# Performance work log

Hardware: AMD Instinct MI355X
Metric: run time of the kernel (lower is better)

## Reference

```python
import jax, jax.numpy as jnp
import numpy as np
from jax import lax

W_BCE, W_DICE, W_FT, W_HD = 1.0, 1.0, 1.0, 0.1
TV_ALPHA, TV_BETA, TV_GAMMA = 0.7, 0.3, 0.75
HD_MAX_DIST, HD_BK = 10, 3
SMOOTH, EPS, HD_EPS = 1e-6, 1e-7, 1e-8


def _max_pool(x, k):
    # torch F.max_pool2d pads with -inf implicitly
    pad = k // 2
    return lax.reduce_window(x, -jnp.inf, lax.max, (1, 1, k, k), (1, 1, 1, 1),
                             [(0, 0), (0, 0), (pad, pad), (pad, pad)])


def _min_pool(x, k):
    pad = k // 2
    return lax.reduce_window(x, jnp.inf, lax.min, (1, 1, k, k), (1, 1, 1, 1),
                             [(0, 0), (0, 0), (pad, pad), (pad, pad)])


def _soft_boundary(mask, k):
    dil = _max_pool(mask, k)
    ero = _min_pool(mask, k)  # == -max_pool(-mask)
    return jnp.maximum(dil - ero, 0.0)


def _bce_with_logits(logits, target):
    # numerically stable: max(x,0) - x*t + log1p(exp(-|x|))
    return jnp.mean(jnp.maximum(logits, 0.0) - logits * target +
                    jnp.log1p(jnp.exp(-jnp.abs(logits))))


def _dice_loss(probs, target):
    p = probs.reshape(probs.shape[0], -1)
    t = target.reshape(target.shape[0], -1)
    inter = jnp.sum(p * t, axis=1)
    denom = jnp.sum(p, axis=1) + jnp.sum(t, axis=1)
    dice = (2.0 * inter + SMOOTH) / (denom + SMOOTH + EPS)
    return jnp.mean(1.0 - dice)


def _focal_tversky(probs, target):
    p = probs.reshape(probs.shape[0], -1)
    t = target.reshape(target.shape[0], -1)
    TP = jnp.sum(p * t, axis=1)
    FP = jnp.sum(p * (1.0 - t), axis=1)
    FN = jnp.sum((1.0 - p) * t, axis=1)
    tv = (TP + SMOOTH) / (TP + TV_ALPHA * FP + TV_BETA * FN + SMOOTH + EPS)
    return jnp.mean(jnp.power(1.0 - tv, TV_GAMMA))


def _hausdorff_surrogate(probs, target):
    pred_b = _soft_boundary(probs, HD_BK)
    gt_b = _soft_boundary(target, HD_BK)
    total = jnp.zeros((), probs.dtype)
    weight_sum = 0.0
    for d in range(1, HD_MAX_DIST + 1):
        pred_d = _max_pool(pred_b, 2 * d + 1)
        gt_d = _max_pool(gt_b, 2 * d + 1)
        w = float(d) / float(HD_MAX_DIST)
        total = total + w * (jnp.mean(jnp.abs(pred_d - gt_b)) +
                             jnp.mean(jnp.abs(gt_d - pred_b)))
        weight_sum += w
    return total / (weight_sum + HD_EPS)


def setup_inputs() -> dict:
    key = jax.random.key(0)
    k1, k2 = jax.random.split(key)
    B, C, H, W = 16, 1, 512, 512
    logits = jax.random.normal(k1, (B, C, H, W), dtype=jnp.float32)
    target = jax.random.randint(k2, (B, C, H, W), 0, 2, dtype=jnp.int32)
    return {"logits": logits, "target": target}


def reference(logits, target):
    t = target.astype(jnp.float32)
    bce = _bce_with_logits(logits, t)
    probs = jax.nn.sigmoid(logits)
    d = _dice_loss(probs, t)
    ft = _focal_tversky(probs, t)
    hd = _hausdorff_surrogate(probs, t)
    return W_BCE * bce + W_DICE * d + W_FT * ft + W_HD * hd
```

## Files before the change

kernel.cpp:

```cpp
#include <hip/hip_runtime.h>
#include <math.h>

namespace {

constexpr int B = 16, H = 512, W = 512;
constexpr int HWc = H * W;
constexpr size_t Nc = (size_t)B * HWc;

constexpr int NSTRIP = 13;
constexpr int CENT = 42;
constexpr int NBAND = 16;
constexpr int NWORK = NSTRIP * NBAND * B * 2;
constexpr int NSB = NWORK / 4;
constexpr int NBCE = B * 64;

template <int CTRL>
__device__ __forceinline__ float dpp_shift1(float v) {
  int i = __float_as_int(v);
  int r = __builtin_amdgcn_update_dpp(i, i, CTRL, 0xF, 0xF, false);
  return __int_as_float(r);
}

__device__ __forceinline__ float hmax3(float v) {
  return fmaxf(fmaxf(dpp_shift1<0x138>(v), v), dpp_shift1<0x130>(v));
}
__device__ __forceinline__ void hminmax3(float v, float& mx, float& mn) {
  float s1 = dpp_shift1<0x138>(v);
  float s2 = dpp_shift1<0x130>(v);
  mx = fmaxf(fmaxf(s1, v), s2);
  mn = fminf(fminf(s1, v), s2);
}

__device__ __forceinline__ float wave_sum(float v) {
#pragma unroll
  for (int off = 32; off > 0; off >>= 1) v += __shfl_down(v, off);
  return v;
}

__device__ __forceinline__ float block_reduce_256(float v, float* sm, int tid) {
#pragma unroll
  for (int off = 32; off > 0; off >>= 1) v += __shfl_down(v, off);
  int lane = tid & 63, wid = tid >> 6;
  if (lane == 0) sm[wid] = v;
  __syncthreads();
  float r = 0.f;
  if (tid == 0) r = sm[0] + sm[1] + sm[2] + sm[3];
  __syncthreads();
  return r;
}

template <int CH>
__device__ __forceinline__ float load_src(const float* __restrict__ Lg,
                                          const int* __restrict__ Tg, int gy,
                                          int colc) {
  gy = min(max(gy, 0), H - 1);
  if constexpr (CH == 0) {
    float x = Lg[gy * W + colc];
    float e = __expf(-x);
    return __builtin_amdgcn_rcpf(1.f + e);
  } else {
    return (float)Tg[gy * W + colc];
  }
}

template <int D>
__device__ __forceinline__ void dilate_steps(float (&a)[52],
                                             const float (&o)[32],
                                             float (&accv)[4]) {
  if constexpr (D <= 10) {
    float hp = hmax3(a[D - 1]);
    float hc = hmax3(a[D]);
#pragma unroll
    for (int r = D; r <= 51 - D; ++r) {
      float hn = hmax3(a[r + 1]);
      float nv = fmaxf(fmaxf(hp, hc), hn);
      hp = hc;
      hc = hn;
      a[r] = nv;
    }
    constexpr float wd = 0.1f * (float)D;
#pragma unroll
    for (int k = 0; k < 32; ++k) accv[k & 3] += wd * fabsf(a[10 + k] - o[k]);
    dilate_steps<D + 1>(a, o, accv);
  }
}

template <int CH>
__device__ __forceinline__ void fused_body(const float* __restrict__ Lg,
                                           const int* __restrict__ Tg,
                                           int lane, int strip, int band,
                                           int bz,
                                           float* __restrict__ chain_p) {
  int col = strip * CENT - 11 + lane;
  int colc = min(max(col, 0), W - 1);
  int y0 = band * 32;

  float o[32];
  {
    float v0 = load_src<1 - CH>(Lg, Tg, y0 - 1, colc);
    float v1 = load_src<1 - CH>(Lg, Tg, y0, colc);
    float hx0, hn0, hx1, hn1;
    hminmax3(v0, hx0, hn0);
    hminmax3(v1, hx1, hn1);
#pragma unroll
    for (int k = 0; k < 32; ++k) {
      float v2 = load_src<1 - CH>(Lg, Tg, y0 + 1 + k, colc);
      float hx2, hn2;
      hminmax3(v2, hx2, hn2);
      o[k] = fmaxf(fmaxf(hx0, hx1), hx2) - fminf(fminf(hn0, hn1), hn2);
      hx0 = hx1;
      hx1 = hx2;
      hn0 = hn1;
      hn1 = hn2;
    }
  }

  float a[52];
  {
    float v0 = load_src<CH>(Lg, Tg, y0 - 11, colc);
    float v1 = load_src<CH>(Lg, Tg, y0 - 10, colc);
    float hx0, hn0, hx1, hn1;
    hminmax3(v0, hx0, hn0);
    hminmax3(v1, hx1, hn1);
#pragma unroll
    for (int r = 0; r < 52; ++r) {
      float v2 = load_src<CH>(Lg, Tg, y0 - 9 + r, colc);
      float hx2, hn2;
      hminmax3(v2, hx2, hn2);
      a[r] = fmaxf(fmaxf(hx0, hx1), hx2) - fminf(fminf(hn0, hn1), hn2);
      hx0 = hx1;
      hx1 = hx2;
      hn0 = hn1;
      hn1 = hn2;
    }
  }

  float accv[4] = {0.f, 0.f, 0.f, 0.f};
  dilate_steps<1>(a, o, accv);
  float acc = (accv[0] + accv[1]) + (accv[2] + accv[3]);

  bool valid = (lane >= 11 && lane <= 52 && col < W);
  acc = valid ? acc : 0.f;
  acc = wave_sum(acc);
  if (lane == 0) chain_p[(bz * NBAND + band) * NSTRIP + strip] = acc;
}

__device__ __forceinline__ void bce_body(const float* __restrict__ logits,
                                         const int* __restrict__ target,
                                         int blk, float* __restrict__ bceA,
                                         float* __restrict__ spA,
                                         float* __restrict__ stA,
                                         float* __restrict__ sptA) {
  __shared__ float smr[4];
  int img = blk >> 6, seg = blk & 63;
  const float4* L4 =
      (const float4*)(logits + (size_t)img * HWc + (size_t)seg * 4096);
  const int4* T4 =
      (const int4*)(target + (size_t)img * HWc + (size_t)seg * 4096);
  int tid = threadIdx.x;
  float s_bce = 0.f, s_p = 0.f, s_t = 0.f, s_pt = 0.f;
#pragma unroll
  for (int it = 0; it < 4; ++it) {
    float4 x4 = L4[it * 256 + tid];
    int4 t4 = T4[it * 256 + tid];
    float xs[4] = {x4.x, x4.y, x4.z, x4.w};
    int ts[4] = {t4.x, t4.y, t4.z, t4.w};
#pragma unroll
    for (int j = 0; j < 4; ++j) {
      float x = xs[j];
      float tf = (float)ts[j];
      float e = __expf(-x);
      float p = __builtin_amdgcn_rcpf(1.f + e);
      s_p += p;
      s_t += tf;
      s_pt += p * tf;
      s_bce += x * (1.f - tf) + __logf(1.f + e);
    }
  }
  float r;
  r = block_reduce_256(s_bce, smr, tid);
  if (tid == 0) bceA[blk] = r;
  r = block_reduce_256(s_p, smr, tid);
  if (tid == 0) spA[blk] = r;
  r = block_reduce_256(s_t, smr, tid);
  if (tid == 0) stA[blk] = r;
  r = block_reduce_256(s_pt, smr, tid);
  if (tid == 0) sptA[blk] = r;
}

__global__ void __launch_bounds__(256, 4) fused_kernel(
    const float* __restrict__ logits, const int* __restrict__ target,
    float* __restrict__ bceA, float* __restrict__ spA,
    float* __restrict__ stA, float* __restrict__ sptA,
    float* __restrict__ chain_p) {
  if (blockIdx.x < NBCE) {
    bce_body(logits, target, blockIdx.x, bceA, spA, stA, sptA);
    return;
  }
  int tid = threadIdx.x;
  int lane = tid & 63;
  int wv = __builtin_amdgcn_readfirstlane(tid >> 6);
  int widx = (blockIdx.x - NBCE) * 4 + wv;
  int strip = widx % NSTRIP;
  int rest = widx / NSTRIP;
  int band = rest & 15;
  int bz = rest >> 4;
  int img = bz & 15, chain = bz >> 4;
  const float* Lg = logits + (size_t)img * HWc;
  const int* Tg = target + (size_t)img * HWc;
  if (chain == 0)
    fused_body<0>(Lg, Tg, lane, strip, band, bz, chain_p);
  else
    fused_body<1>(Lg, Tg, lane, strip, band, bz, chain_p);
}

__global__ void finalize_kernel(const float* __restrict__ bceA,
                                const float* __restrict__ spA,
                                const float* __restrict__ stA,
                                const float* __restrict__ sptA,
                                const float* __restrict__ chain_p,
                                float* __restrict__ out) {
  __shared__ float smr[4];
  __shared__ float smImg[16][3];
  __shared__ double smd[16][2];
  int tid = threadIdx.x;

  float s = 0.f;
  for (int i = tid; i < NBCE; i += 256) s += bceA[i];
  float bce_sum = block_reduce_256(s, smr, tid);

  s = 0.f;
  for (int i = tid; i < NWORK; i += 256) s += chain_p[i];
  float hd_sum = block_reduce_256(s, smr, tid);

  {
    int img = tid >> 4, part = tid & 15;
    float sp = 0.f, st = 0.f, spt = 0.f;
    for (int j = part; j < 64; j += 16) {
      int idx = img * 64 + j;
      sp += spA[idx];
      st += stA[idx];
      spt += sptA[idx];
    }
#pragma unroll
    for (int off = 8; off > 0; off >>= 1) {
      sp += __shfl_down(sp, off, 16);
      st += __shfl_down(st, off, 16);
      spt += __shfl_down(spt, off, 16);
    }
    if (part == 0) {
      smImg[img][0] = sp;
      smImg[img][1] = st;
      smImg[img][2] = spt;
    }
  }
  __syncthreads();
  if (tid < 16) {
    double sp = smImg[tid][0], st = smImg[tid][1], spt = smImg[tid][2];
    double dice = (2.0 * spt + 1e-6) / (sp + st + 1e-6 + 1e-7);
    double tv = (spt + 1e-6) /
                (spt + 0.7 * (sp - spt) + 0.3 * (st - spt) + 1e-6 + 1e-7);
    smd[tid][0] = 1.0 - dice;
    smd[tid][1] = pow(1.0 - tv, 0.75);
  }
  __syncthreads();
  if (tid == 0) {
    double dice_l = 0.0, ft_l = 0.0;
    for (int i = 0; i < 16; ++i) {
      dice_l += smd[i][0];
      ft_l += smd[i][1];
    }
    dice_l /= 16.0;
    ft_l /= 16.0;
    const double Nd = (double)Nc;
    double bce = (double)bce_sum / Nd;
    double hd = ((double)hd_sum / Nd) / (5.5 + 1e-8);
    out[0] = (float)(bce + dice_l + ft_l + 0.1 * hd);
  }
}

}

extern "C" void kernel_launch(void* const* d_in, const int* in_sizes, int n_in,
                              void* d_out, int out_size, void* d_ws,
                              size_t ws_size, hipStream_t stream) {
  const float* logits = (const float*)d_in[0];
  const int* target = (const int*)d_in[1];
  float* out = (float*)d_out;

  float* part = (float*)d_ws;
  float* bceA = part;
  float* spA = part + NBCE;
  float* stA = part + 2 * NBCE;
  float* sptA = part + 3 * NBCE;
  float* chain_p = part + 4 * NBCE;

  fused_kernel<<<dim3(NBCE + NSB), dim3(256), 0, stream>>>(
      logits, target, bceA, spA, stA, sptA, chain_p);
  finalize_kernel<<<1, 256, 0, stream>>>(bceA, spA, stA, sptA, chain_p, out);
}
```

Before: 136.6 us.

## Use bit-packed binary morphology for target boundary dilation chain

Measured after the change: 119.4 us. 1.14x faster.

```diff
diff --git a/kernel.cpp b/kernel.cpp
--- a/kernel.cpp
+++ b/kernel.cpp
@@ -14,12 +14,18 @@
 constexpr int NSB = NWORK / 4;
 constexpr int NBCE = B * 64;
 
+
 template <int CTRL>
 __device__ __forceinline__ float dpp_shift1(float v) {
   int i = __float_as_int(v);
   int r = __builtin_amdgcn_update_dpp(i, i, CTRL, 0xF, 0xF, false);
   return __int_as_float(r);
 }
+template <int CTRL>
+__device__ __forceinline__ unsigned dpp_shift1u(unsigned v) {
+  return (unsigned)__builtin_amdgcn_update_dpp((int)v, (int)v, CTRL, 0xF, 0xF,
+                                               false);
+}
 
 __device__ __forceinline__ float hmax3(float v) {
   return fmaxf(fmaxf(dpp_shift1<0x138>(v), v), dpp_shift1<0x130>(v));
@@ -29,6 +35,19 @@
   float s2 = dpp_shift1<0x130>(v);
   mx = fmaxf(fmaxf(s1, v), s2);
   mn = fminf(fminf(s1, v), s2);
+}
+
+__device__ __forceinline__ unsigned long long or3_lanes(unsigned long long v) {
+  unsigned lo = (unsigned)v, hi = (unsigned)(v >> 32);
+  unsigned rlo = dpp_shift1u<0x138>(lo) | lo | dpp_shift1u<0x130>(lo);
+  unsigned rhi = dpp_shift1u<0x138>(hi) | hi | dpp_shift1u<0x130>(hi);
+  return ((unsigned long long)rhi << 32) | rlo;
+}
+__device__ __forceinline__ unsigned long long and3_lanes(unsigned long long v) {
+  unsigned lo = (unsigned)v, hi = (unsigned)(v >> 32);
+  unsigned rlo = dpp_shift1u<0x138>(lo) & lo & dpp_shift1u<0x130>(lo);
+  unsigned rhi = dpp_shift1u<0x138>(hi) & hi & dpp_shift1u<0x130>(hi);
+  return ((unsigned long long)rhi << 32) | rlo;
 }
 
 __device__ __forceinline__ float wave_sum(float v) {
@@ -85,26 +104,25 @@
   }
 }
 
-template <int CH>
-__device__ __forceinline__ void fused_body(const float* __restrict__ Lg,
-                                           const int* __restrict__ Tg,
-                                           int lane, int strip, int band,
-                                           int bz,
-                                           float* __restrict__ chain_p) {
+__device__ __forceinline__ void fused_body0(const float* __restrict__ Lg,
+                                            const int* __restrict__ Tg,
+                                            int lane, int strip, int band,
+                                            int bz,
+                                            float* __restrict__ chain_p) {
   int col = strip * CENT - 11 + lane;
   int colc = min(max(col, 0), W - 1);
   int y0 = band * 32;
 
   float o[32];
   {
-    float v0 = load_src<1 - CH>(Lg, Tg, y0 - 1, colc);
-    float v1 = load_src<1 - CH>(Lg, Tg, y0, colc);
+    float v0 = load_src<1>(Lg, Tg, y0 - 1, colc);
+    float v1 = load_src<1>(Lg, Tg, y0, colc);
     float hx0, hn0, hx1, hn1;
     hminmax3(v0, hx0, hn0);
     hminmax3(v1, hx1, hn1);
 #pragma unroll
     for (int k = 0; k < 32; ++k) {
-      float v2 = load_src<1 - CH>(Lg, Tg, y0 + 1 + k, colc);
+      float v2 = load_src<1>(Lg, Tg, y0 + 1 + k, colc);
       float hx2, hn2;
       hminmax3(v2, hx2, hn2);
       o[k] = fmaxf(fmaxf(hx0, hx1), hx2) - fminf(fminf(hn0, hn1), hn2);
@@ -117,14 +135,14 @@
 
   float a[52];
   {
-    float v0 = load_src<CH>(Lg, Tg, y0 - 11, colc);
-    float v1 = load_src<CH>(Lg, Tg, y0 - 10, colc);
+    float v0 = load_src<0>(Lg, Tg, y0 - 11, colc);
+    float v1 = load_src<0>(Lg, Tg, y0 - 10, colc);
     float hx0, hn0, hx1, hn1;
     hminmax3(v0, hx0, hn0);
     hminmax3(v1, hx1, hn1);
 #pragma unroll
     for (int r = 0; r < 52; ++r) {
-      float v2 = load_src<CH>(Lg, Tg, y0 - 9 + r, colc);
+      float v2 = load_src<0>(Lg, Tg, y0 - 9 + r, colc);
       float hx2, hn2;
       hminmax3(v2, hx2, hn2);
       a[r] = fmaxf(fmaxf(hx0, hx1), hx2) - fminf(fminf(hn0, hn1), hn2);
@@ -145,13 +163,74 @@
   if (lane == 0) chain_p[(bz * NBAND + band) * NSTRIP + strip] = acc;
 }
 
+__device__ __forceinline__ void fused_body1(const float* __restrict__ Lg,
+                                            const int* __restrict__ Tg,
+                                            int lane, int strip, int band,
+                                            int bz,
+                                            float* __restrict__ chain_p) {
+  int col = strip * CENT - 11 + lane;
+  int colc = min(max(col, 0), W - 1);
+  int y0 = band * 32;
+
+  float o[32];
+  {
+    float v0 = load_src<0>(Lg, Tg, y0 - 1, colc);
+    float v1 = load_src<0>(Lg, Tg, y0, colc);
+    float hx0, hn0, hx1, hn1;
+    hminmax3(v0, hx0, hn0);
+    hminmax3(v1, hx1, hn1);
+#pragma unroll
+    for (int k = 0; k < 32; ++k) {
+      float v2 = load_src<0>(Lg, Tg, y0 + 1 + k, colc);
+      float hx2, hn2;
+      hminmax3(v2, hx2, hn2);
+      o[k] = fmaxf(fmaxf(hx0, hx1), hx2) - fminf(fminf(hn0, hn1), hn2);
+      hx0 = hx1;
+      hx1 = hx2;
+      hn0 = hn1;
+      hn1 = hn2;
+    }
+  }
+
+  unsigned long long tb = 0ull;
+#pragma unroll
+  for (int j = 0; j < 54; ++j) {
+    int gy = min(max(y0 - 11 + j, 0), H - 1);
+    tb |= (unsigned long long)(unsigned)Tg[gy * W + colc] << j;
+  }
+
+  unsigned long long vd = tb | (tb << 1) | (tb >> 1);
+  unsigned long long ve = tb & (tb << 1) & (tb >> 1);
+  unsigned long long ab = (or3_lanes(vd) & ~and3_lanes(ve)) >> 1;
+
+  float accv[4] = {0.f, 0.f, 0.f, 0.f};
+#pragma unroll
+  for (int d = 1; d <= 10; ++d) {
+    unsigned long long s = ab | (ab << 1) | (ab >> 1);
+    ab = or3_lanes(s);
+    const float wd = 0.1f * (float)d;
+    unsigned lo = (unsigned)ab, hi = (unsigned)(ab >> 32);
+#pragma unroll
+    for (int k = 0; k < 32; ++k) {
+      unsigned bit =
+          (k < 22) ? ((lo >> (10 + k)) & 1u) : ((hi >> (k - 22)) & 1u);
+      accv[k & 3] += wd * fabsf((float)bit - o[k]);
+    }
+  }
+  float acc = (accv[0] + accv[1]) + (accv[2] + accv[3]);
+
+  bool valid = (lane >= 11 && lane <= 52 && col < W);
+  acc = valid ? acc : 0.f;
+  acc = wave_sum(acc);
+  if (lane == 0) chain_p[(bz * NBAND + band) * NSTRIP + strip] = acc;
+}
+
 __device__ __forceinline__ void bce_body(const float* __restrict__ logits,
                                          const int* __restrict__ target,
                                          int blk, float* __restrict__ bceA,
                                          float* __restrict__ spA,
                                          float* __restrict__ stA,
-                                         float* __restrict__ sptA) {
-  __shared__ float smr[4];
+                                         float* __restrict__ sptA, float* sm) {
   int img = blk >> 6, seg = blk & 63;
   const float4* L4 =
       (const float4*)(logits + (size_t)img * HWc + (size_t)seg * 4096);
@@ -178,13 +257,13 @@
     }
   }
   float r;
-  r = block_reduce_256(s_bce, smr, tid);
+  r = block_reduce_256(s_bce, sm, tid);
   if (tid == 0) bceA[blk] = r;
-  r = block_reduce_256(s_p, smr, tid);
+  r = block_reduce_256(s_p, sm, tid);
   if (tid == 0) spA[blk] = r;
-  r = block_reduce_256(s_t, smr, tid);
+  r = block_reduce_256(s_t, sm, tid);
   if (tid == 0) stA[blk] = r;
-  r = block_reduce_256(s_pt, smr, tid);
+  r = block_reduce_256(s_pt, sm, tid);
   if (tid == 0) sptA[blk] = r;
 }
 
@@ -193,11 +272,12 @@
     float* __restrict__ bceA, float* __restrict__ spA,
     float* __restrict__ stA, float* __restrict__ sptA,
     float* __restrict__ chain_p) {
+  __shared__ float smr[4];
+  int tid = threadIdx.x;
   if (blockIdx.x < NBCE) {
-    bce_body(logits, target, blockIdx.x, bceA, spA, stA, sptA);
+    bce_body(logits, target, blockIdx.x, bceA, spA, stA, sptA, smr);
     return;
   }
-  int tid = threadIdx.x;
   int lane = tid & 63;
   int wv = __builtin_amdgcn_readfirstlane(tid >> 6);
   int widx = (blockIdx.x - NBCE) * 4 + wv;
@@ -209,9 +289,9 @@
   const float* Lg = logits + (size_t)img * HWc;
   const int* Tg = target + (size_t)img * HWc;
   if (chain == 0)
-    fused_body<0>(Lg, Tg, lane, strip, band, bz, chain_p);
+    fused_body0(Lg, Tg, lane, strip, band, bz, chain_p);
   else
-    fused_body<1>(Lg, Tg, lane, strip, band, bz, chain_p);
+    fused_body1(Lg, Tg, lane, strip, band, bz, chain_p);
 }
 
 __global__ void finalize_kernel(const float* __restrict__ bceA,
@@ -226,11 +306,23 @@
   int tid = threadIdx.x;
 
   float s = 0.f;
-  for (int i = tid; i < NBCE; i += 256) s += bceA[i];
+  {
+    const float4* b4 = (const float4*)bceA;
+    for (int i = tid; i < NBCE / 4; i += 256) {
+      float4 v = b4[i];
+      s += (v.x + v.y) + (v.z + v.w);
+    }
+  }
   float bce_sum = block_reduce_256(s, smr, tid);
 
   s = 0.f;
-  for (int i = tid; i < NWORK; i += 256) s += chain_p[i];
+  {
+    const float4* c4 = (const float4*)chain_p;
+    for (int i = tid; i < NWORK / 4; i += 256) {
+      float4 v = c4[i];
+      s += (v.x + v.y) + (v.z + v.w);
+    }
+  }
   float hd_sum = block_reduce_256(s, smr, tid);
 
   {
```
